# Performance work log

Measured on AMD Instinct MI355X. Metric: run time of the kernel, lower is better.

The kernel has to match this reference:

```python
import jax, jax.numpy as jnp
import numpy as np

# Per-type input feature dims (NODE_DIM values); max dim = 128 = padded width of x.
NODE_DIMS = np.array([16, 32, 64, 128, 64, 32, 16, 128], dtype=np.int32)
N_TYPES = 8
MAX_DIM = 128
FEAT = 256          # node_feature_dim
N_GRAPHS = 100000   # batch_size; one node of each type per graph


def setup_inputs() -> dict:
    key = jax.random.key(0)
    k1, k2, k3 = jax.random.split(key, 3)
    num_nodes = N_GRAPHS * N_TYPES
    x = jax.random.normal(k1, (num_nodes, MAX_DIM), dtype=jnp.float32)
    # Per-type Linear weights, padded to MAX_DIM on the input axis.
    W = jax.random.normal(k2, (N_TYPES, FEAT, MAX_DIM), dtype=jnp.float32) * 0.05
    b = jax.random.normal(k3, (N_TYPES, FEAT), dtype=jnp.float32) * 0.05
    return {"x": x, "W": W, "b": b}


def reference(x, W, b):
    # Node n = g*N_TYPES + k is the type-k node of graph g (the gather index
    # ptr[b] + node_name.index(k) in the original). Dropout is eval-mode (identity).
    # Mask weight columns beyond each type's true input dim: equivalent to
    # slicing x[:, :NODE_DIM[k]] before the per-type Linear.
    mask = (jnp.arange(MAX_DIM)[None, None, :] < jnp.asarray(NODE_DIMS)[:, None, None]).astype(x.dtype)  # [T,1,D]
    W_eff = W * mask  # [T,F,D]
    xg = x.reshape(N_GRAPHS, N_TYPES, MAX_DIM)  # [G,T,D]
    y = jnp.einsum("gtd,tfd->gtf", xg, W_eff) + b[None, :, :]  # [G,T,F]
    return y.reshape(N_GRAPHS * N_TYPES, FEAT)
```

## Files before the change

### kernel.cpp

```cpp
#include <hip/hip_runtime.h>

#define N_GRAPHS 100000
#define NTYPES 8
#define MAXD 128
#define FEAT 256
#define ALDA 136
#define ELDA 68

typedef __attribute__((ext_vector_type(8))) short short8;
typedef __attribute__((ext_vector_type(4))) float f32x4;
typedef __attribute__((ext_vector_type(4))) unsigned uint4v;

constexpr int KSN[NTYPES]  = {1, 1, 2, 4, 2, 1, 1, 4};
constexpr int DIMS[NTYPES] = {16, 32, 64, 128, 64, 32, 16, 128};

__device__ __forceinline__ unsigned f2bf_u(float f) {
    unsigned u = __builtin_bit_cast(unsigned, f);
    return (u + 0x7fffu + ((u >> 16) & 1u)) >> 16;
}
__device__ __forceinline__ unsigned cvt2(float lo, float hi) {
    return f2bf_u(lo) | (f2bf_u(hi) << 16);
}
__device__ __forceinline__ short8 cvt8(f32x4 a, f32x4 b) {
    uint4v u;
    u.x = cvt2(a.x, a.y); u.y = cvt2(a.z, a.w);
    u.z = cvt2(b.x, b.y); u.w = cvt2(b.z, b.w);
    return __builtin_bit_cast(short8, u);
}

__global__ __launch_bounds__(256)
void prepack_w(const float* __restrict__ W, short8* __restrict__ wp)
{
    const int idx  = blockIdx.x * 256 + threadIdx.x;
    const int c16  = idx & 15;
    const int cgrp = (idx >> 4) & 3;
    const int ks   = (idx >> 6) & 3;
    const int ct   = (idx >> 8) & 15;
    const int t    = (idx >> 12) & 7;
    const int col  = ct * 16 + c16;
    const int k    = ks * 32 + cgrp * 8;
    const int dim  = 16 << ((0x30123210u >> (4 * t)) & 0xf);
    const float* src = W + ((size_t)t * FEAT + col) * MAXD + k;
    f32x4 a = *(const f32x4*)src;
    f32x4 b = *(const f32x4*)(src + 4);
    #pragma unroll
    for (int j = 0; j < 4; ++j) {
        if (k + j     >= dim) a[j] = 0.f;
        if (k + 4 + j >= dim) b[j] = 0.f;
    }
    wp[idx] = cvt8(a, b);
}

template<int T, bool PRE>
__device__ __forceinline__ void do_type(const float* __restrict__ x,
                                        const short8* __restrict__ wp,
                                        const float* __restrict__ W,
                                        const float* __restrict__ bias_g,
                                        float* __restrict__ out,
                                        unsigned short* __restrict__ as_,
                                        float* __restrict__ ep,
                                        int g0, int lane, int cgrp, int c16)
{
    constexpr int KS   = KSN[T];
    constexpr int K32  = KS * 32;
    constexpr int SPR8 = K32 / 8;
    constexpr int PASSES = 16 * SPR8 / 64;

    #pragma unroll
    for (int p = 0; p < PASSES; ++p) {
        const int idx = p * 64 + lane;
        const int row = idx / SPR8;
        const int s8  = idx % SPR8;
        const float* rp = x + (((size_t)(g0 + row)) * NTYPES + T) * MAXD + s8 * 8;
        f32x4 v0 = __builtin_nontemporal_load((const f32x4*)rp);
        f32x4 v1 = __builtin_nontemporal_load((const f32x4*)rp + 1);
        *(short8*)&as_[row * ALDA + s8 * 8] = cvt8(v0, v1);
    }

    short8 a[KS];
    #pragma unroll
    for (int ks = 0; ks < KS; ++ks)
        a[ks] = *(const short8*)&as_[c16 * ALDA + ks * 32 + cgrp * 8];

    #pragma unroll
    for (int ct4 = 0; ct4 < 4; ++ct4) {
        #pragma unroll
        for (int c = 0; c < 4; ++c) {
            const int ct = ct4 * 4 + c;
            short8 wf[KS];
            if constexpr (PRE) {
                #pragma unroll
                for (int ks = 0; ks < KS; ++ks)
                    wf[ks] = wp[(((T * 16 + ct) * 4 + ks) * 4 + cgrp) * 16 + c16];
            } else {
                constexpr int DIM = DIMS[T];
                #pragma unroll
                for (int ks = 0; ks < KS; ++ks) {
                    const int k = ks * 32 + cgrp * 8;
                    const float* wfp = W + ((size_t)T * FEAT + ct * 16 + c16) * MAXD + k;
                    f32x4 wa = *(const f32x4*)wfp;
                    f32x4 wb = *(const f32x4*)(wfp + 4);
                    #pragma unroll
                    for (int j = 0; j < 4; ++j) {
                        if (k + j     >= DIM) wa[j] = 0.f;
                        if (k + 4 + j >= DIM) wb[j] = 0.f;
                    }
                    wf[ks] = cvt8(wa, wb);
                }
            }
            f32x4 acc = {0.f, 0.f, 0.f, 0.f};
            #pragma unroll
            for (int ks = 0; ks < KS; ++ks)
                acc = __builtin_amdgcn_mfma_f32_16x16x32_bf16(a[ks], wf[ks], acc, 0, 0, 0);
            #pragma unroll
            for (int r = 0; r < 4; ++r)
                ep[(cgrp * 4 + r) * ELDA + (ct & 3) * 16 + c16] = acc[r];
        }
        #pragma unroll
        for (int i = 0; i < 4; ++i) {
            const int row   = i * 4 + (lane >> 4);
            const int coldw = (lane & 15) * 4;
            f32x4 v  = *(const f32x4*)&ep[row * ELDA + coldw];
            f32x4 b4 = *(const f32x4*)&bias_g[T * FEAT + ct4 * 64 + coldw];
            f32x4 res;
            #pragma unroll
            for (int r = 0; r < 4; ++r) res[r] = v[r] + b4[r];
            __builtin_nontemporal_store(res,
                (f32x4*)&out[(((size_t)(g0 + row)) * NTYPES + T) * FEAT + ct4 * 64 + coldw]);
        }
    }

    if constexpr (T + 1 < NTYPES)
        do_type<T + 1, PRE>(x, wp, W, bias_g, out, as_, ep, g0, lane, cgrp, c16);
}

template<bool PRE>
__global__ __launch_bounds__(256, 3)
void node_enc(const float* __restrict__ x, const short8* __restrict__ wp,
              const float* __restrict__ W, const float* __restrict__ bias_g,
              float* __restrict__ out)
{
    __shared__ __align__(16) unsigned short As[4][16 * ALDA];
    __shared__ __align__(16) float          Ep[4][16 * ELDA];
    const int tid  = threadIdx.x;
    const int lane = tid & 63;
    const int wave = tid >> 6;
    const int cgrp = lane >> 4;
    const int c16  = lane & 15;
    const int g0   = blockIdx.x * 64 + wave * 16;
    if (g0 >= N_GRAPHS) return;

    do_type<0, PRE>(x, wp, W, bias_g, out, As[wave], Ep[wave], g0, lane, cgrp, c16);
}

extern "C" void kernel_launch(void* const* d_in, const int* in_sizes, int n_in,
                              void* d_out, int out_size, void* d_ws, size_t ws_size,
                              hipStream_t stream)
{
    const float* x = (const float*)d_in[0];
    const float* W = (const float*)d_in[1];
    const float* b = (const float*)d_in[2];
    float* out = (float*)d_out;

    const int grid = (N_GRAPHS + 63) / 64;
    const size_t wp_bytes = (size_t)32768 * sizeof(short8);

    if (ws_size >= wp_bytes) {
        short8* wp = (short8*)d_ws;
        prepack_w<<<128, 256, 0, stream>>>(W, wp);
        node_enc<true><<<grid, 256, 0, stream>>>(x, wp, W, b, out);
    } else {
        node_enc<false><<<grid, 256, 0, stream>>>(x, nullptr, W, b, out);
    }
}
```

Baseline: 281.7 us.

## Process two 16-graph blocks per wave and load A fragments directly to registers

Each wave now handles 32 graphs instead of 16, reusing each loaded weight fragment across two MFMA row blocks. Input rows are loaded straight from global memory into MFMA register fragments, dropping the LDS staging buffer for A. Occupancy hint is raised to 4 blocks per SM. This trades register pressure and less-coalesced input loads for less weight traffic, fewer LDS round-trips and fewer blocks.

```diff
diff --git a/kernel.cpp b/kernel.cpp
--- a/kernel.cpp
+++ b/kernel.cpp
@@ -4,7 +4,9 @@
 #define NTYPES 8
 #define MAXD 128
 #define FEAT 256
-#define ALDA 136
+#define NB 2
+#define GPW (16 * NB)
+#define GPB (GPW * 4)
 #define ELDA 68
 
 typedef __attribute__((ext_vector_type(8))) short short8;
@@ -57,30 +59,23 @@
                                         const float* __restrict__ W,
                                         const float* __restrict__ bias_g,
                                         float* __restrict__ out,
-                                        unsigned short* __restrict__ as_,
                                         float* __restrict__ ep,
                                         int g0, int lane, int cgrp, int c16)
 {
-    constexpr int KS   = KSN[T];
-    constexpr int K32  = KS * 32;
-    constexpr int SPR8 = K32 / 8;
-    constexpr int PASSES = 16 * SPR8 / 64;
+    constexpr int KS = KSN[T];
 
+    short8 a[NB][KS];
     #pragma unroll
-    for (int p = 0; p < PASSES; ++p) {
-        const int idx = p * 64 + lane;
-        const int row = idx / SPR8;
-        const int s8  = idx % SPR8;
-        const float* rp = x + (((size_t)(g0 + row)) * NTYPES + T) * MAXD + s8 * 8;
-        f32x4 v0 = __builtin_nontemporal_load((const f32x4*)rp);
-        f32x4 v1 = __builtin_nontemporal_load((const f32x4*)rp + 1);
-        *(short8*)&as_[row * ALDA + s8 * 8] = cvt8(v0, v1);
+    for (int b = 0; b < NB; ++b) {
+        const size_t grow = (size_t)(g0 + b * 16 + c16) * NTYPES + T;
+        #pragma unroll
+        for (int ks = 0; ks < KS; ++ks) {
+            const float* rp = x + grow * MAXD + ks * 32 + cgrp * 8;
+            f32x4 v0 = __builtin_nontemporal_load((const f32x4*)rp);
+            f32x4 v1 = __builtin_nontemporal_load((const f32x4*)rp + 1);
+            a[b][ks] = cvt8(v0, v1);
+        }
     }
-
-    short8 a[KS];
-    #pragma unroll
-    for (int ks = 0; ks < KS; ++ks)
-        a[ks] = *(const short8*)&as_[c16 * ALDA + ks * 32 + cgrp * 8];
 
     #pragma unroll
     for (int ct4 = 0; ct4 < 4; ++ct4) {
@@ -108,16 +103,19 @@
                     wf[ks] = cvt8(wa, wb);
                 }
             }
-            f32x4 acc = {0.f, 0.f, 0.f, 0.f};
             #pragma unroll
-            for (int ks = 0; ks < KS; ++ks)
-                acc = __builtin_amdgcn_mfma_f32_16x16x32_bf16(a[ks], wf[ks], acc, 0, 0, 0);
-            #pragma unroll
-            for (int r = 0; r < 4; ++r)
-                ep[(cgrp * 4 + r) * ELDA + (ct & 3) * 16 + c16] = acc[r];
+            for (int b = 0; b < NB; ++b) {
+                f32x4 acc = {0.f, 0.f, 0.f, 0.f};
+                #pragma unroll
+                for (int ks = 0; ks < KS; ++ks)
+                    acc = __builtin_amdgcn_mfma_f32_16x16x32_bf16(a[b][ks], wf[ks], acc, 0, 0, 0);
+                #pragma unroll
+                for (int r = 0; r < 4; ++r)
+                    ep[(b * 16 + cgrp * 4 + r) * ELDA + c * 16 + c16] = acc[r];
+            }
         }
         #pragma unroll
-        for (int i = 0; i < 4; ++i) {
+        for (int i = 0; i < 8; ++i) {
             const int row   = i * 4 + (lane >> 4);
             const int coldw = (lane & 15) * 4;
             f32x4 v  = *(const f32x4*)&ep[row * ELDA + coldw];
@@ -131,26 +129,25 @@
     }
 
     if constexpr (T + 1 < NTYPES)
-        do_type<T + 1, PRE>(x, wp, W, bias_g, out, as_, ep, g0, lane, cgrp, c16);
+        do_type<T + 1, PRE>(x, wp, W, bias_g, out, ep, g0, lane, cgrp, c16);
 }
 
 template<bool PRE>
-__global__ __launch_bounds__(256, 3)
+__global__ __launch_bounds__(256, 4)
 void node_enc(const float* __restrict__ x, const short8* __restrict__ wp,
               const float* __restrict__ W, const float* __restrict__ bias_g,
               float* __restrict__ out)
 {
-    __shared__ __align__(16) unsigned short As[4][16 * ALDA];
-    __shared__ __align__(16) float          Ep[4][16 * ELDA];
+    __shared__ __align__(16) float Ep[4][GPW * ELDA];
     const int tid  = threadIdx.x;
     const int lane = tid & 63;
     const int wave = tid >> 6;
     const int cgrp = lane >> 4;
     const int c16  = lane & 15;
-    const int g0   = blockIdx.x * 64 + wave * 16;
+    const int g0   = blockIdx.x * GPB + wave * GPW;
     if (g0 >= N_GRAPHS) return;
 
-    do_type<0, PRE>(x, wp, W, bias_g, out, As[wave], Ep[wave], g0, lane, cgrp, c16);
+    do_type<0, PRE>(x, wp, W, bias_g, out, Ep[wave], g0, lane, cgrp, c16);
 }
 
 extern "C" void kernel_launch(void* const* d_in, const int* in_sizes, int n_in,
@@ -162,7 +159,7 @@
     const float* b = (const float*)d_in[2];
     float* out = (float*)d_out;
 
-    const int grid = (N_GRAPHS + 63) / 64;
+    const int grid = (N_GRAPHS + GPB - 1) / GPB;
     const size_t wp_bytes = (size_t)32768 * sizeof(short8);
 
     if (ws_size >= wp_bytes) {
```

Measured after the change: 296.8 us. 5.3% more time.

## Prefetch next node type's x rows into registers during current type's MFMA work

Applied to the files above, without the earlier changes.

Software-pipelines the per-type loop. Global loads of the next type's x tile are issued into registers before the current type's MFMA and output phase. They are converted to bf16 and written to LDS only after that phase ends, so global load latency overlaps compute and stores. The type-0 tile is loaded in the kernel prologue. This raises register pressure (up to 8 extra float4 per lane), which could reduce occupancy under the 3-blocks launch bound.

```diff
diff --git a/kernel.cpp b/kernel.cpp
--- a/kernel.cpp
+++ b/kernel.cpp
@@ -61,20 +61,21 @@
                                         float* __restrict__ ep,
                                         int g0, int lane, int cgrp, int c16)
 {
-    constexpr int KS   = KSN[T];
-    constexpr int K32  = KS * 32;
-    constexpr int SPR8 = K32 / 8;
-    constexpr int PASSES = 16 * SPR8 / 64;
+    constexpr int KS  = KSN[T];
+    constexpr int NXT = (T + 1 < NTYPES) ? T + 1 : T;
+    constexpr int KSn = KSN[NXT];
+    constexpr int SPRn = KSn * 4;
 
-    #pragma unroll
-    for (int p = 0; p < PASSES; ++p) {
-        const int idx = p * 64 + lane;
-        const int row = idx / SPR8;
-        const int s8  = idx % SPR8;
-        const float* rp = x + (((size_t)(g0 + row)) * NTYPES + T) * MAXD + s8 * 8;
-        f32x4 v0 = __builtin_nontemporal_load((const f32x4*)rp);
-        f32x4 v1 = __builtin_nontemporal_load((const f32x4*)rp + 1);
-        *(short8*)&as_[row * ALDA + s8 * 8] = cvt8(v0, v1);
+    f32x4 pv[2 * KSn];
+    if constexpr (T + 1 < NTYPES) {
+        #pragma unroll
+        for (int p = 0; p < KSn; ++p) {
+            const int idx = p * 64 + lane;
+            const int row = idx / SPRn, s8 = idx % SPRn;
+            const float* rp = x + (((size_t)(g0 + row)) * NTYPES + (T + 1)) * MAXD + s8 * 8;
+            pv[2 * p]     = __builtin_nontemporal_load((const f32x4*)rp);
+            pv[2 * p + 1] = __builtin_nontemporal_load((const f32x4*)rp + 1);
+        }
     }
 
     short8 a[KS];
@@ -130,8 +131,15 @@
         }
     }
 
-    if constexpr (T + 1 < NTYPES)
+    if constexpr (T + 1 < NTYPES) {
+        #pragma unroll
+        for (int p = 0; p < KSn; ++p) {
+            const int idx = p * 64 + lane;
+            const int row = idx / SPRn, s8 = idx % SPRn;
+            *(short8*)&as_[row * ALDA + s8 * 8] = cvt8(pv[2 * p], pv[2 * p + 1]);
+        }
         do_type<T + 1, PRE>(x, wp, W, bias_g, out, as_, ep, g0, lane, cgrp, c16);
+    }
 }
 
 template<bool PRE>
@@ -150,7 +158,16 @@
     const int g0   = blockIdx.x * 64 + wave * 16;
     if (g0 >= N_GRAPHS) return;
 
-    do_type<0, PRE>(x, wp, W, bias_g, out, As[wave], Ep[wave], g0, lane, cgrp, c16);
+    unsigned short* as_ = As[wave];
+    {
+        const int row = lane >> 2, s8 = lane & 3;
+        const float* rp = x + (((size_t)(g0 + row)) * NTYPES + 0) * MAXD + s8 * 8;
+        f32x4 v0 = __builtin_nontemporal_load((const f32x4*)rp);
+        f32x4 v1 = __builtin_nontemporal_load((const f32x4*)rp + 1);
+        *(short8*)&as_[row * ALDA + s8 * 8] = cvt8(v0, v1);
+    }
+
+    do_type<0, PRE>(x, wp, W, bias_g, out, as_, Ep[wave], g0, lane, cgrp, c16);
 }
 
 extern "C" void kernel_launch(void* const* d_in, const int* in_sizes, int n_in,
```

Measured after the change: 279.2 us. No clear change (-0.9%).
